# Performance work log

Hardware: AMD Instinct MI355X
Metric: run time of the kernel (lower is better)

Reference implementation:

```python
import jax, jax.numpy as jnp
import numpy as np

VOCAB = 50257
EMB = 100
BOT = 5  # bottleneck dim of the tiny autoencoder MLP


def setup_inputs() -> dict:
    key = jax.random.key(0)
    ks = jax.random.split(key, 7)
    B, S = 128, 2048
    x = jax.random.randint(ks[0], (B, S), 0, VOCAB, dtype=jnp.int64)
    word_embed = jax.random.normal(ks[1], (VOCAB, EMB), dtype=jnp.float32)
    # idf values are positive; use uniform(0,1] scaled up a bit to mimic log-idf
    idf = jax.random.uniform(ks[2], (VOCAB,), dtype=jnp.float32, minval=0.01, maxval=10.0)
    fc1_w = jax.random.normal(ks[3], (BOT, EMB), dtype=jnp.float32) * (1.0 / np.sqrt(EMB))
    fc1_b = jax.random.normal(ks[4], (BOT,), dtype=jnp.float32) * 0.01
    fc2_w = jax.random.normal(ks[5], (EMB, BOT), dtype=jnp.float32) * (1.0 / np.sqrt(BOT))
    fc2_b = jax.random.normal(ks[6], (EMB,), dtype=jnp.float32) * 0.01
    return {"x": x, "word_embed": word_embed, "idf": idf,
            "fc1_w": fc1_w, "fc1_b": fc1_b, "fc2_w": fc2_w, "fc2_b": fc2_b}


def reference(x, word_embed, idf, fc1_w, fc1_b, fc2_w, fc2_b):
    B, S = x.shape
    V = idf.shape[0]
    # tf(): per-row token histogram. Equivalent math to the torch dense
    # one-hot scatter + sum over seq, done as a scatter-add (no (B,S,V) tensor).
    rows = jnp.broadcast_to(jnp.arange(B)[:, None], (B, S))
    tf = jnp.zeros((B, V), dtype=jnp.float32).at[rows, x].add(1.0)
    # tf-idf weights, row-normalized
    tfidf = tf * idf[None, :]
    tfidf = tfidf / jnp.sum(tfidf, axis=1, keepdims=True)
    # per-token weight: gather each row's tfidf at its token ids  -> [B, S]
    w = jnp.take_along_axis(tfidf, x, axis=1)
    # embedding lookup and tfidf-weighted sum over seq  -> [B, EMB]
    emb = word_embed[x]  # [B, S, EMB]
    doc = jnp.einsum('bse,bs->be', emb, w)
    # tiny 100 -> 5 -> 100 MLP (no nonlinearity in the original)
    h = doc @ fc1_w.T + fc1_b
    out = h @ fc2_w.T + fc2_b
    return out
```

## Files before the change

### kernel.cpp

```cpp
#include <hip/hip_runtime.h>

#define SEQ 2048
#define EMB 100
#define BOT 5
#define HSIZE 4096
#define SPLIT 32
#define K1T 1024

__global__ __launch_bounds__(K1T) void k1_hist(
    const int* __restrict__ x, const float* __restrict__ idf,
    float* __restrict__ coef)
{
    __shared__ int   hkey[HSIZE];
    __shared__ int   hcnt[HSIZE];
    __shared__ float red[K1T / 64];
    __shared__ float zinv;

    const int b = blockIdx.x, tid = threadIdx.x;
    const int lane = tid & 63, wid = tid >> 6;

    for (int i = tid; i < HSIZE; i += K1T) { hkey[i] = -1; hcnt[i] = 0; }
    __syncthreads();

    const int* xrow = x + (size_t)b * SEQ;

    int   mykey[SEQ / K1T];
    float myidf[SEQ / K1T];
    float z = 0.0f;
    #pragma unroll
    for (int j = 0; j < SEQ / K1T; ++j) {
        int s   = tid + j * K1T;
        int key = xrow[s];
        float w = idf[key];
        mykey[j] = key;
        myidf[j] = w;
        z += w;
        unsigned slot = ((unsigned)key * 2654435761u) >> 20;
        for (;;) {
            int prev = atomicCAS(&hkey[slot], -1, key);
            if (prev == -1 || prev == key) { atomicAdd(&hcnt[slot], 1); break; }
            slot = (slot + 1) & (HSIZE - 1);
        }
    }
    for (int off = 32; off > 0; off >>= 1) z += __shfl_down(z, off);
    if (lane == 0) red[wid] = z;
    __syncthreads();
    if (tid == 0) {
        float t = 0.0f;
        #pragma unroll
        for (int i = 0; i < K1T / 64; ++i) t += red[i];
        zinv = 1.0f / t;
    }
    __syncthreads();
    const float iz = zinv;

    #pragma unroll
    for (int j = 0; j < SEQ / K1T; ++j) {
        int s   = tid + j * K1T;
        int key = mykey[j];
        unsigned slot = ((unsigned)key * 2654435761u) >> 20;
        while (hkey[slot] != key) slot = (slot + 1) & (HSIZE - 1);
        coef[(size_t)b * SEQ + s] = (float)hcnt[slot] * myidf[j] * iz;
    }
}

__global__ __launch_bounds__(256) void k2_gather(
    const int* __restrict__ x, const float* __restrict__ coef,
    const float* __restrict__ we, float* __restrict__ partial)
{
    __shared__ int   skey[SEQ];
    __shared__ float scoef[SEQ];
    __shared__ float part[2][EMB];

    const int bx  = blockIdx.x;
    const int b   = bx / SPLIT;
    const int sp  = bx % SPLIT;
    const int tid = threadIdx.x;
    const int g   = tid >> 7;
    const int e   = tid & 127;

    const int*   kk = x    + (size_t)b * SEQ;
    const float* cc = coef + (size_t)b * SEQ;
    for (int i = tid; i < SEQ; i += 256) { skey[i] = kk[i]; scoef[i] = cc[i]; }
    __syncthreads();

    const int st = SPLIT * 2;
    if (e < EMB) {
        float a0 = 0, a1 = 0, a2 = 0, a3 = 0, a4 = 0, a5 = 0, a6 = 0, a7 = 0;
        int i = sp * 2 + g;
        for (; i + 7 * st < SEQ; i += 8 * st) {
            int   k0 = skey[i],        k1 = skey[i + st],     k2 = skey[i + 2*st], k3 = skey[i + 3*st];
            int   k4 = skey[i + 4*st], k5 = skey[i + 5*st],   k6 = skey[i + 6*st], k7 = skey[i + 7*st];
            float c0 = scoef[i],        c1 = scoef[i + st],   c2 = scoef[i + 2*st], c3 = scoef[i + 3*st];
            float c4 = scoef[i + 4*st], c5 = scoef[i + 5*st], c6 = scoef[i + 6*st], c7 = scoef[i + 7*st];
            a0 += c0 * we[(size_t)k0 * EMB + e];
            a1 += c1 * we[(size_t)k1 * EMB + e];
            a2 += c2 * we[(size_t)k2 * EMB + e];
            a3 += c3 * we[(size_t)k3 * EMB + e];
            a4 += c4 * we[(size_t)k4 * EMB + e];
            a5 += c5 * we[(size_t)k5 * EMB + e];
            a6 += c6 * we[(size_t)k6 * EMB + e];
            a7 += c7 * we[(size_t)k7 * EMB + e];
        }
        for (; i < SEQ; i += st) a0 += scoef[i] * we[(size_t)skey[i] * EMB + e];
        part[g][e] = ((a0 + a1) + (a2 + a3)) + ((a4 + a5) + (a6 + a7));
    }
    __syncthreads();
    if (tid < EMB) partial[(size_t)bx * EMB + tid] = part[0][tid] + part[1][tid];
}

__global__ __launch_bounds__(128) void k3_mlp(
    const float* __restrict__ partial,
    const float* __restrict__ fc1w, const float* __restrict__ fc1b,
    const float* __restrict__ fc2w, const float* __restrict__ fc2b,
    float* __restrict__ out)
{
    __shared__ float doc[EMB];
    __shared__ float hsh[BOT];

    const int b = blockIdx.x, tid = threadIdx.x;

    if (tid < EMB) {
        float a = 0.0f;
        const float* p = partial + (size_t)b * SPLIT * EMB + tid;
        #pragma unroll
        for (int s = 0; s < SPLIT; ++s) a += p[s * EMB];
        doc[tid] = a;
    }
    __syncthreads();

    if (tid < BOT) {
        float h = fc1b[tid];
        const float* wr = fc1w + tid * EMB;
        for (int e = 0; e < EMB; ++e) h += doc[e] * wr[e];
        hsh[tid] = h;
    }
    __syncthreads();

    if (tid < EMB) {
        float o = fc2b[tid];
        const float* wr = fc2w + tid * BOT;
        #pragma unroll
        for (int j = 0; j < BOT; ++j) o += hsh[j] * wr[j];
        out[(size_t)b * EMB + tid] = o;
    }
}

extern "C" void kernel_launch(void* const* d_in, const int* in_sizes, int n_in,
                              void* d_out, int out_size, void* d_ws, size_t ws_size,
                              hipStream_t stream) {
    const int*   x    = (const int*)d_in[0];
    const float* we   = (const float*)d_in[1];
    const float* idf  = (const float*)d_in[2];
    const float* fc1w = (const float*)d_in[3];
    const float* fc1b = (const float*)d_in[4];
    const float* fc2w = (const float*)d_in[5];
    const float* fc2b = (const float*)d_in[6];
    float*       out  = (float*)d_out;

    const int B = in_sizes[0] / SEQ;

    char* ws = (char*)d_ws;
    float* coef    = (float*)ws;
    float* partial = (float*)(ws + (size_t)B * SEQ * 4);

    k1_hist  <<<B,         K1T, 0, stream>>>(x, idf, coef);
    k2_gather<<<B * SPLIT, 256, 0, stream>>>(x, coef, we, partial);
    k3_mlp   <<<B,         128, 0, stream>>>(partial, fc1w, fc1b, fc2w, fc2b, out);
}
```

Baseline: 106.9 us.

## Restructure gather kernel: contiguous chunks per block, float2 row loads, fewer splits

```diff
diff --git a/kernel.cpp b/kernel.cpp
--- a/kernel.cpp
+++ b/kernel.cpp
@@ -4,7 +4,8 @@
 #define EMB 100
 #define BOT 5
 #define HSIZE 4096
-#define SPLIT 32
+#define SPLIT 16
+#define CHUNK (SEQ / SPLIT)
 #define K1T 1024
 
 __global__ __launch_bounds__(K1T) void k1_hist(
@@ -68,45 +69,61 @@
     const int* __restrict__ x, const float* __restrict__ coef,
     const float* __restrict__ we, float* __restrict__ partial)
 {
-    __shared__ int   skey[SEQ];
-    __shared__ float scoef[SEQ];
-    __shared__ float part[2][EMB];
+    __shared__ int   skey[CHUNK];
+    __shared__ float scoef[CHUNK];
+    __shared__ float part[4][EMB];
 
-    const int bx  = blockIdx.x;
-    const int b   = bx / SPLIT;
-    const int sp  = bx % SPLIT;
-    const int tid = threadIdx.x;
-    const int g   = tid >> 7;
-    const int e   = tid & 127;
+    const int bx   = blockIdx.x;
+    const int b    = bx >> 4;
+    const int sp   = bx & (SPLIT - 1);
+    const int tid  = threadIdx.x;
+    const int wave = tid >> 6;
+    const int lane = tid & 63;
 
-    const int*   kk = x    + (size_t)b * SEQ;
-    const float* cc = coef + (size_t)b * SEQ;
-    for (int i = tid; i < SEQ; i += 256) { skey[i] = kk[i]; scoef[i] = cc[i]; }
+    const int base = sp * CHUNK;
+    if (tid < CHUNK) {
+        skey [tid] = x   [(size_t)b * SEQ + base + tid];
+        scoef[tid] = coef[(size_t)b * SEQ + base + tid];
+    }
     __syncthreads();
 
-    const int st = SPLIT * 2;
-    if (e < EMB) {
-        float a0 = 0, a1 = 0, a2 = 0, a3 = 0, a4 = 0, a5 = 0, a6 = 0, a7 = 0;
-        int i = sp * 2 + g;
-        for (; i + 7 * st < SEQ; i += 8 * st) {
-            int   k0 = skey[i],        k1 = skey[i + st],     k2 = skey[i + 2*st], k3 = skey[i + 3*st];
-            int   k4 = skey[i + 4*st], k5 = skey[i + 5*st],   k6 = skey[i + 6*st], k7 = skey[i + 7*st];
-            float c0 = scoef[i],        c1 = scoef[i + st],   c2 = scoef[i + 2*st], c3 = scoef[i + 3*st];
-            float c4 = scoef[i + 4*st], c5 = scoef[i + 5*st], c6 = scoef[i + 6*st], c7 = scoef[i + 7*st];
-            a0 += c0 * we[(size_t)k0 * EMB + e];
-            a1 += c1 * we[(size_t)k1 * EMB + e];
-            a2 += c2 * we[(size_t)k2 * EMB + e];
-            a3 += c3 * we[(size_t)k3 * EMB + e];
-            a4 += c4 * we[(size_t)k4 * EMB + e];
-            a5 += c5 * we[(size_t)k5 * EMB + e];
-            a6 += c6 * we[(size_t)k6 * EMB + e];
-            a7 += c7 * we[(size_t)k7 * EMB + e];
+    if (lane < EMB / 2) {
+        float2 a0 = {0,0}, a1 = {0,0}, a2 = {0,0}, a3 = {0,0};
+        float2 a4 = {0,0}, a5 = {0,0}, a6 = {0,0}, a7 = {0,0};
+        const int t0 = wave * 32;
+        #pragma unroll
+        for (int it = 0; it < 4; ++it) {
+            const int i = t0 + it * 8;
+            int   k0 = skey[i+0], k1 = skey[i+1], k2 = skey[i+2], k3 = skey[i+3];
+            int   k4 = skey[i+4], k5 = skey[i+5], k6 = skey[i+6], k7 = skey[i+7];
+            float c0 = scoef[i+0], c1 = scoef[i+1], c2 = scoef[i+2], c3 = scoef[i+3];
+            float c4 = scoef[i+4], c5 = scoef[i+5], c6 = scoef[i+6], c7 = scoef[i+7];
+            float2 v0 = ((const float2*)(we + (size_t)k0 * EMB))[lane];
+            float2 v1 = ((const float2*)(we + (size_t)k1 * EMB))[lane];
+            float2 v2 = ((const float2*)(we + (size_t)k2 * EMB))[lane];
+            float2 v3 = ((const float2*)(we + (size_t)k3 * EMB))[lane];
+            float2 v4 = ((const float2*)(we + (size_t)k4 * EMB))[lane];
+            float2 v5 = ((const float2*)(we + (size_t)k5 * EMB))[lane];
+            float2 v6 = ((const float2*)(we + (size_t)k6 * EMB))[lane];
+            float2 v7 = ((const float2*)(we + (size_t)k7 * EMB))[lane];
+            a0.x += c0 * v0.x; a0.y += c0 * v0.y;
+            a1.x += c1 * v1.x; a1.y += c1 * v1.y;
+            a2.x += c2 * v2.x; a2.y += c2 * v2.y;
+            a3.x += c3 * v3.x; a3.y += c3 * v3.y;
+            a4.x += c4 * v4.x; a4.y += c4 * v4.y;
+            a5.x += c5 * v5.x; a5.y += c5 * v5.y;
+            a6.x += c6 * v6.x; a6.y += c6 * v6.y;
+            a7.x += c7 * v7.x; a7.y += c7 * v7.y;
         }
-        for (; i < SEQ; i += st) a0 += scoef[i] * we[(size_t)skey[i] * EMB + e];
-        part[g][e] = ((a0 + a1) + (a2 + a3)) + ((a4 + a5) + (a6 + a7));
+        float sx = ((a0.x + a1.x) + (a2.x + a3.x)) + ((a4.x + a5.x) + (a6.x + a7.x));
+        float sy = ((a0.y + a1.y) + (a2.y + a3.y)) + ((a4.y + a5.y) + (a6.y + a7.y));
+        part[wave][2 * lane]     = sx;
+        part[wave][2 * lane + 1] = sy;
     }
     __syncthreads();
-    if (tid < EMB) partial[(size_t)bx * EMB + tid] = part[0][tid] + part[1][tid];
+    if (tid < EMB)
+        partial[(size_t)bx * EMB + tid] =
+            (part[0][tid] + part[1][tid]) + (part[2][tid] + part[3][tid]);
 }
 
 __global__ __launch_bounds__(128) void k3_mlp(
```

New measurement: 103.3 us. 1.03x faster.
